# Kernel optimization log

Measured on AMD Instinct MI355X. Metric: run time of the kernel, lower is better.

Reference implementation:

```python
import jax, jax.numpy as jnp
import numpy as np

TEM = 6  # forward hardcodes Tem=6 for index building; init default Tem=6 for weights


def _build_index(H, W, Tem):
    # Faithful port of _build_matrix_index: row edges per phase, col edges per phase,
    # then cross-phase edges linking corresponding pixels of adjacent phases.
    raw = jnp.arange(W, dtype=jnp.int32)[None, :] + jnp.arange(H, dtype=jnp.int32)[:, None] * W  # [H,W]
    pw = W // Tem
    phases = [raw[:, i * pw:(i + 1) * pw] for i in range(Tem)]
    rows = [jnp.stack([p[:-1, :], p[1:, :]], axis=2).reshape(-1, 2) for p in phases]
    cols = [jnp.stack([p[:, :-1], p[:, 1:]], axis=2).reshape(-1, 2) for p in phases]
    cross = [jnp.stack([phases[i], phases[i + 1]], axis=2).reshape(-1, 2) for i in range(Tem - 1)]
    return jnp.concatenate(rows + cols + cross, axis=0)  # [E,2]


def _build_weight_norm2(fm, Tem):
    # Faithful port of _build_feature_weight_norm2_distance, INCLUDING the original
    # per-phase [row,col] interleaved ordering (which differs from the index ordering).
    B, D, H, W = fm.shape
    pw = W // Tem
    phases = [fm[:, :, :, i * pw:(i + 1) * pw] for i in range(Tem)]
    ws = []
    for p in phases:
        wr = ((p[:, :, :-1, :] - p[:, :, 1:, :]) ** 2).sum(axis=1).reshape(B, -1)
        wc = ((p[:, :, :, :-1] - p[:, :, :, 1:]) ** 2).sum(axis=1).reshape(B, -1)
        ws.extend([wr, wc])
    for i in range(Tem - 1):
        ws.append(((phases[i] - phases[i + 1]) ** 2).sum(axis=1).reshape(B, -1))
    return jnp.concatenate(ws, axis=1)  # [B,E]


def _mst_single(u, v, w, V):
    # Vectorized Boruvka MST with pointer-jumping union-find (jit-compatible,
    # fixed round count >= ceil(log2 V)). Ties broken by a globally unique edge rank.
    E = u.shape[0]
    order = jnp.argsort(w)  # stable -> unique rank per edge
    rank = jnp.zeros(E, jnp.int32).at[order].set(jnp.arange(E, dtype=jnp.int32))
    n_rounds = int(np.ceil(np.log2(max(V, 2)))) + 1
    idx_v = jnp.arange(V, dtype=jnp.int32)

    def round_fn(carry, _):
        comp, mask = carry
        cu, cv = comp[u], comp[v]
        active = cu != cv
        key = jnp.where(active, rank, E)  # E = sentinel 'no edge'
        mk = jnp.minimum(jax.ops.segment_min(key, cu, num_segments=V),
                         jax.ops.segment_min(key, cv, num_segments=V))  # min rank per component
        has = mk < E
        sel = order[jnp.clip(mk, 0, E - 1)]  # chosen edge index per component
        a, b = cu[sel], cv[sel]
        other = jnp.where(a == idx_v, b, a)
        parent = jnp.where(has, other, idx_v)
        # break mutual 2-cycles: smaller-index component becomes root
        gp = parent[parent]
        parent = jnp.where((gp == idx_v) & (idx_v < parent), idx_v, parent)
        # full path compression via pointer jumping
        parent = jax.lax.while_loop(lambda p: jnp.any(p[p] != p), lambda p: p[p], parent)
        comp = parent[comp]
        mask = mask.at[jnp.where(has, sel, E)].set(True)  # slot E is scratch
        return (comp, mask), None

    comp0 = jnp.arange(V, dtype=jnp.int32)
    mask0 = jnp.zeros(E + 1, dtype=bool)
    (comp, mask), _ = jax.lax.scan(round_fn, (comp0, mask0), None, length=n_rounds)
    mask = mask[:E]
    # grid graph is connected -> exactly V-1 selected edges; emit sorted edge ids
    tree = jnp.sort(jnp.where(mask, jnp.arange(E, dtype=jnp.int32), E))[: V - 1]
    return tree  # [V-1] int32


def setup_inputs() -> dict:
    key = jax.random.key(0)
    guide_in = jax.random.normal(key, (4, 64, 288, 432), dtype=jnp.float32)
    return {"guide_in": guide_in}


def reference(guide_in):
    B, C, H, W = guide_in.shape
    V = H * W
    index = _build_index(H, W, TEM)  # [E,2], same for every batch element
    weight = _build_weight_norm2(guide_in, TEM)  # [B,E]
    u, v = index[:, 0], index[:, 1]
    tree = jax.vmap(lambda ww: _mst_single(u, v, ww, V))(weight)  # [B, V-1]
    return tree
```

## Files before the change

kernel.cpp:

```cpp
#include <hip/hip_runtime.h>
#include <cstdint>
#include <cstddef>

#define NB 4
#define NC 64
#define HH 288
#define WW 432
#define PW 72
#define NV (HH*WW)
#define R_PER ((HH-1)*PW)
#define C_PER (HH*(PW-1))
#define X_PER (HH*PW)
#define PAIRW (R_PER + C_PER)
#define ROWS_TOT (6*R_PER)
#define ROWCOL (6*PAIRW)
#define NE (ROWCOL + 5*X_PER)
#define NTREE (NV-1)
#define NROUNDS 18
#define CHUNK 4096
#define NCHUNK ((NE + CHUNK - 1)/CHUNK)

typedef unsigned long long ull;

__device__ __forceinline__ void index_uv(int e, int& u, int& v) {
    if (e < ROWS_TOT) {
        int t = e / R_PER, l = e - t * R_PER;
        int h = l / PW, x = l - h * PW;
        u = h * WW + t * PW + x; v = u + WW;
    } else if (e < ROWCOL) {
        int q = e - ROWS_TOT;
        int t = q / C_PER, l = q - t * C_PER;
        int h = l / (PW-1), x = l - h * (PW-1);
        u = h * WW + t * PW + x; v = u + 1;
    } else {
        int q = e - ROWCOL;
        int t = q / X_PER, l = q - t * X_PER;
        int h = l / PW, x = l - h * PW;
        u = h * WW + t * PW + x; v = u + PW;
    }
}

__device__ __forceinline__ void weight_uv(int e, int& a, int& b) {
    if (e < ROWCOL) {
        int t = e / PAIRW, r = e - t * PAIRW;
        if (r < R_PER) {
            int h = r / PW, x = r - h * PW;
            a = h * WW + t * PW + x; b = a + WW;
        } else {
            int r2 = r - R_PER;
            int h = r2 / (PW-1), x = r2 - h * (PW-1);
            a = h * WW + t * PW + x; b = a + 1;
        }
    } else {
        int q = e - ROWCOL;
        int t = q / X_PER, l = q - t * X_PER;
        int h = l / PW, x = l - h * PW;
        a = h * WW + t * PW + x; b = a + PW;
    }
}

__device__ __forceinline__ int rootOf(const int* __restrict__ par, int c) {
    while (true) {
        int p = par[c];
        if (p == c) return c;
        int pp = par[p];
        if (pp == c) return c < p ? c : p;
        c = p;
    }
}

__global__ __launch_bounds__(256) void init_kernel(int* comp, int* parent,
                                                   ull* minkey, unsigned char* mask,
                                                   unsigned char* alive,
                                                   int* foundA, int* foundB, int* done) {
    int i = blockIdx.x * 256 + threadIdx.x;
    int b = blockIdx.y;
    if (i < NV) {
        comp[(size_t)b*NV + i] = i;
        parent[(size_t)b*NV + i] = i;
        minkey[(size_t)b*NV + i] = ~0ULL;
    }
    if (i < NE) {
        mask[(size_t)b*NE + i] = 0;
        alive[(size_t)b*NE + i] = 1;
    }
    if (i == 0) { foundA[b] = 0; foundB[b] = 0; done[b] = 0; }
}

__global__ __launch_bounds__(256) void key_kernel(const float* __restrict__ fm,
                                                  ull* __restrict__ keys) {
    int e = blockIdx.x * 256 + threadIdx.x;
    int b = blockIdx.y;
    if (e >= NE) return;
    int a, c2;
    weight_uv(e, a, c2);
    const float* base = fm + (size_t)b * NC * NV;
    float w = 0.f;
    #pragma unroll 8
    for (int ch = 0; ch < NC; ++ch) {
        float d = base[(size_t)ch * NV + a] - base[(size_t)ch * NV + c2];
        w += d * d;
    }
    keys[(size_t)b * NE + e] =
        ((ull)__float_as_uint(w) << 32) | (unsigned int)e;
}

__global__ __launch_bounds__(256) void scan_kernel(const ull* __restrict__ keys,
                                                   int* __restrict__ comp,
                                                   const int* __restrict__ parent,
                                                   ull* __restrict__ minkey,
                                                   unsigned char* __restrict__ alive,
                                                   int* __restrict__ foundCur,
                                                   const int* __restrict__ done) {
    int e = blockIdx.x * 256 + threadIdx.x;
    int b = blockIdx.y;
    if (e >= NE) return;
    if (done[b]) return;
    if (!alive[(size_t)b * NE + e]) return;
    const int* par = parent + (size_t)b * NV;
    int* cmp = comp + (size_t)b * NV;
    int u, v;
    index_uv(e, u, v);
    int cu = rootOf(par, cmp[u]);
    if (cmp[u] != cu) cmp[u] = cu;
    int cv = rootOf(par, cmp[v]);
    if (cmp[v] != cv) cmp[v] = cv;
    bool pred = (cu != cv);
    if (!pred) alive[(size_t)b * NE + e] = 0;
    ull m = __ballot(pred ? 1 : 0);
    if (m && (threadIdx.x & 63) == (unsigned)(__ffsll((long long)m) - 1))
        foundCur[b] = 1;
    if (pred) {
        ull k = keys[(size_t)b * NE + e];
        ull* mk = minkey + (size_t)b * NV;
        if (k < mk[cu]) atomicMin(&mk[cu], k);
        if (k < mk[cv]) atomicMin(&mk[cv], k);
    }
}

__global__ __launch_bounds__(256) void select_kernel(const int* __restrict__ comp,
                                                     int* __restrict__ parent,
                                                     ull* __restrict__ minkey,
                                                     unsigned char* __restrict__ mask,
                                                     const int* __restrict__ foundCur,
                                                     int* __restrict__ foundNext,
                                                     int* __restrict__ done) {
    int c = blockIdx.x * 256 + threadIdx.x;
    int b = blockIdx.y;
    int fc = foundCur[b];
    if (c == 0) {
        foundNext[b] = 0;
        if (fc == 0) done[b] = 1;
    }
    if (fc == 0) return;
    if (c >= NV) return;
    size_t off = (size_t)b * NV;
    ull k = minkey[off + c];
    int par = c;
    if (k != ~0ULL) {
        minkey[off + c] = ~0ULL;
        int e = (int)(k & 0xffffffffu);
        mask[(size_t)b * NE + e] = 1;
        int u, v;
        index_uv(e, u, v);
        int cu = comp[off + u], cv = comp[off + v];
        par = (cu == c) ? cv : cu;
    }
    if (parent[off + c] != par) parent[off + c] = par;
}

__global__ __launch_bounds__(256) void count_kernel(const unsigned char* __restrict__ mask,
                                                    int* __restrict__ counts) {
    int b = blockIdx.y, ck = blockIdx.x, t = threadIdx.x;
    const unsigned char* m = mask + (size_t)b * NE;
    int base_e = ck * CHUNK + t * 16;
    int cnt = 0;
    #pragma unroll
    for (int i = 0; i < 16; ++i) {
        int e = base_e + i;
        if (e < NE && m[e]) cnt++;
    }
    __shared__ int sh[256];
    sh[t] = cnt;
    __syncthreads();
    for (int o = 128; o > 0; o >>= 1) {
        if (t < o) sh[t] += sh[t + o];
        __syncthreads();
    }
    if (t == 0) counts[b * NCHUNK + ck] = sh[0];
}

__global__ void offs_kernel(const int* __restrict__ counts, int* __restrict__ offsets) {
    int b = threadIdx.x;
    if (b >= NB) return;
    int run = 0;
    for (int ck = 0; ck < NCHUNK; ++ck) {
        int c = counts[b * NCHUNK + ck];
        offsets[b * NCHUNK + ck] = run;
        run += c;
    }
}

__global__ __launch_bounds__(256) void write_kernel(const unsigned char* __restrict__ mask,
                                                    const int* __restrict__ offsets,
                                                    int* __restrict__ out) {
    int b = blockIdx.y, ck = blockIdx.x, t = threadIdx.x;
    const unsigned char* m = mask + (size_t)b * NE;
    int base_e = ck * CHUNK + t * 16;
    int cnt = 0;
    #pragma unroll
    for (int i = 0; i < 16; ++i) {
        int e = base_e + i;
        if (e < NE && m[e]) cnt++;
    }
    __shared__ int sh[256];
    sh[t] = cnt;
    __syncthreads();
    for (int o = 1; o < 256; o <<= 1) {
        int v = 0;
        if (t >= o) v = sh[t - o];
        __syncthreads();
        sh[t] += v;
        __syncthreads();
    }
    int pos = offsets[b * NCHUNK + ck] + (sh[t] - cnt);
    for (int i = 0; i < 16; ++i) {
        int e = base_e + i;
        if (e < NE && m[e]) {
            if (pos < NTREE) out[(size_t)b * NTREE + pos] = e;
            pos++;
        }
    }
}

extern "C" void kernel_launch(void* const* d_in, const int* in_sizes, int n_in,
                              void* d_out, int out_size, void* d_ws, size_t ws_size,
                              hipStream_t stream) {
    const float* fm = (const float*)d_in[0];
    int* out = (int*)d_out;

    char* ws = (char*)d_ws;
    size_t off = 0;
    auto alloc = [&](size_t bytes) -> void* {
        void* p = ws + off;
        off += (bytes + 255) & ~(size_t)255;
        return p;
    };
    ull* keys    = (ull*)alloc((size_t)NB * NE * 8);
    ull* minkey  = (ull*)alloc((size_t)NB * NV * 8);
    int* comp    = (int*)alloc((size_t)NB * NV * 4);
    int* parent  = (int*)alloc((size_t)NB * NV * 4);
    unsigned char* mask  = (unsigned char*)alloc((size_t)NB * NE);
    unsigned char* alive = (unsigned char*)alloc((size_t)NB * NE);
    int* counts  = (int*)alloc((size_t)NB * NCHUNK * 4);
    int* offsets = (int*)alloc((size_t)NB * NCHUNK * 4);
    int* foundA  = (int*)alloc(NB * 4);
    int* foundB  = (int*)alloc(NB * 4);
    int* done    = (int*)alloc(NB * 4);

    dim3 blk(256);
    dim3 gE((NE + 255) / 256, NB);
    dim3 gV((NV + 255) / 256, NB);

    init_kernel<<<gE, blk, 0, stream>>>(comp, parent, minkey, mask, alive,
                                        foundA, foundB, done);
    key_kernel<<<gE, blk, 0, stream>>>(fm, keys);

    for (int r = 0; r < NROUNDS; ++r) {
        int* fCur  = (r & 1) ? foundB : foundA;
        int* fNext = (r & 1) ? foundA : foundB;
        scan_kernel<<<gE, blk, 0, stream>>>(keys, comp, parent, minkey, alive,
                                            fCur, done);
        select_kernel<<<gV, blk, 0, stream>>>(comp, parent, minkey, mask,
                                              fCur, fNext, done);
    }

    count_kernel<<<dim3(NCHUNK, NB), blk, 0, stream>>>(mask, counts);
    offs_kernel<<<1, NB, 0, stream>>>(counts, offsets);
    write_kernel<<<dim3(NCHUNK, NB), blk, 0, stream>>>(mask, offsets, out);
}
```

Measured before the change: 667.4 us.

## Compute edge weights per pixel, fuse first Boruvka scan, bitpack alive flags

The edge-weight kernel now runs once per pixel instead of once per edge, computing the vertical, horizontal and cross-phase distances from one shared center load. This cuts redundant reads of the 64-channel feature map. The same kernel atomically seeds the per-component minimum keys, which replaces the first scan round. The alive flags move from bytes to 32-bit bitmasks written once per wavefront, and the separate offsets kernel is folded into write_kernel as a per-block reduction over the chunk counts. The trade-off is more atomics in the key kernel and a redundant reduction of the counts in every write block.

```diff
diff --git a/kernel.cpp b/kernel.cpp
--- a/kernel.cpp
+++ b/kernel.cpp
@@ -17,6 +17,7 @@
 #define NE (ROWCOL + 5*X_PER)
 #define NTREE (NV-1)
 #define NROUNDS 18
+#define NWORDS ((NE + 31)/32)
 #define CHUNK 4096
 #define NCHUNK ((NE + CHUNK - 1)/CHUNK)
 
@@ -40,25 +41,6 @@
     }
 }
 
-__device__ __forceinline__ void weight_uv(int e, int& a, int& b) {
-    if (e < ROWCOL) {
-        int t = e / PAIRW, r = e - t * PAIRW;
-        if (r < R_PER) {
-            int h = r / PW, x = r - h * PW;
-            a = h * WW + t * PW + x; b = a + WW;
-        } else {
-            int r2 = r - R_PER;
-            int h = r2 / (PW-1), x = r2 - h * (PW-1);
-            a = h * WW + t * PW + x; b = a + 1;
-        }
-    } else {
-        int q = e - ROWCOL;
-        int t = q / X_PER, l = q - t * X_PER;
-        int h = l / PW, x = l - h * PW;
-        a = h * WW + t * PW + x; b = a + PW;
-    }
-}
-
 __device__ __forceinline__ int rootOf(const int* __restrict__ par, int c) {
     while (true) {
         int p = par[c];
@@ -71,8 +53,8 @@
 
 __global__ __launch_bounds__(256) void init_kernel(int* comp, int* parent,
                                                    ull* minkey, unsigned char* mask,
-                                                   unsigned char* alive,
-                                                   int* foundA, int* foundB, int* done) {
+                                                   unsigned* aliveW,
+                                                   int* found, int* done) {
     int i = blockIdx.x * 256 + threadIdx.x;
     int b = blockIdx.y;
     if (i < NV) {
@@ -80,62 +62,99 @@
         parent[(size_t)b*NV + i] = i;
         minkey[(size_t)b*NV + i] = ~0ULL;
     }
-    if (i < NE) {
-        mask[(size_t)b*NE + i] = 0;
-        alive[(size_t)b*NE + i] = 1;
-    }
-    if (i == 0) { foundA[b] = 0; foundB[b] = 0; done[b] = 0; }
-}
-
-__global__ __launch_bounds__(256) void key_kernel(const float* __restrict__ fm,
-                                                  ull* __restrict__ keys) {
-    int e = blockIdx.x * 256 + threadIdx.x;
-    int b = blockIdx.y;
-    if (e >= NE) return;
-    int a, c2;
-    weight_uv(e, a, c2);
-    const float* base = fm + (size_t)b * NC * NV;
-    float w = 0.f;
+    if (i < NE) mask[(size_t)b*NE + i] = 0;
+    if (i < NWORDS) aliveW[(size_t)b*NWORDS + i] = 0xffffffffu;
+    if (b == 0 && i < NB) { found[i] = 1; found[NB + i] = 0; done[i] = 0; }
+}
+
+__global__ __launch_bounds__(256) void key0_kernel(const float* __restrict__ fm,
+                                                   ull* __restrict__ keys,
+                                                   ull* __restrict__ minkey) {
+    int i = blockIdx.x * 256 + threadIdx.x;
+    int b = blockIdx.y;
+    if (i >= NV) return;
+    int h = i / WW, x = i - h * WW;
+    int t = x / PW, xr = x - t * PW;
+    bool hv = (h < HH-1);
+    bool hh = (xr < PW-1);
+    bool hx = (x < WW-PW);
+    int ov = hv ? WW : 0;
+    int oh = hh ? 1  : 0;
+    int ox = hx ? PW : 0;
+    const float* base = fm + (size_t)b * NC * NV + i;
+    float sv = 0.f, sh_ = 0.f, sx = 0.f;
     #pragma unroll 8
     for (int ch = 0; ch < NC; ++ch) {
-        float d = base[(size_t)ch * NV + a] - base[(size_t)ch * NV + c2];
-        w += d * d;
-    }
-    keys[(size_t)b * NE + e] =
-        ((ull)__float_as_uint(w) << 32) | (unsigned int)e;
+        const float* p = base + (size_t)ch * NV;
+        float f0 = p[0];
+        float dv = f0 - p[ov];
+        float dh = f0 - p[oh];
+        float dx = f0 - p[ox];
+        sv += dv * dv; sh_ += dh * dh; sx += dx * dx;
+    }
+    ull* mk = minkey + (size_t)b * NV;
+    ull* ky = keys + (size_t)b * NE;
+    if (hv) {
+        int e = t * PAIRW + h * PW + xr;
+        ull k = ((ull)__float_as_uint(sv) << 32) | (unsigned int)e;
+        ky[e] = k;
+        int u, v; index_uv(e, u, v);
+        atomicMin(&mk[u], k); atomicMin(&mk[v], k);
+    }
+    if (hh) {
+        int e = t * PAIRW + R_PER + h * (PW-1) + xr;
+        ull k = ((ull)__float_as_uint(sh_) << 32) | (unsigned int)e;
+        ky[e] = k;
+        int u, v; index_uv(e, u, v);
+        atomicMin(&mk[u], k); atomicMin(&mk[v], k);
+    }
+    if (hx) {
+        int e = ROWCOL + t * X_PER + h * PW + xr;
+        ull k = ((ull)__float_as_uint(sx) << 32) | (unsigned int)e;
+        ky[e] = k;
+        int u, v; index_uv(e, u, v);
+        atomicMin(&mk[u], k); atomicMin(&mk[v], k);
+    }
 }
 
 __global__ __launch_bounds__(256) void scan_kernel(const ull* __restrict__ keys,
                                                    int* __restrict__ comp,
                                                    const int* __restrict__ parent,
                                                    ull* __restrict__ minkey,
-                                                   unsigned char* __restrict__ alive,
+                                                   unsigned* __restrict__ aliveW,
                                                    int* __restrict__ foundCur,
                                                    const int* __restrict__ done) {
     int e = blockIdx.x * 256 + threadIdx.x;
     int b = blockIdx.y;
-    if (e >= NE) return;
     if (done[b]) return;
-    if (!alive[(size_t)b * NE + e]) return;
-    const int* par = parent + (size_t)b * NV;
-    int* cmp = comp + (size_t)b * NV;
-    int u, v;
-    index_uv(e, u, v);
-    int cu = rootOf(par, cmp[u]);
-    if (cmp[u] != cu) cmp[u] = cu;
-    int cv = rootOf(par, cmp[v]);
-    if (cmp[v] != cv) cmp[v] = cv;
-    bool pred = (cu != cv);
-    if (!pred) alive[(size_t)b * NE + e] = 0;
-    ull m = __ballot(pred ? 1 : 0);
-    if (m && (threadIdx.x & 63) == (unsigned)(__ffsll((long long)m) - 1))
-        foundCur[b] = 1;
-    if (pred) {
+    const int lane = threadIdx.x & 63;
+    unsigned* aw = aliveW + (size_t)b * NWORDS;
+    bool was = false, live = false;
+    int cu = 0, cv = 0;
+    if (e < NE) was = (aw[e >> 5] >> (e & 31)) & 1;
+    if (was) {
+        const int* par = parent + (size_t)b * NV;
+        int* cmp = comp + (size_t)b * NV;
+        int u, v; index_uv(e, u, v);
+        cu = rootOf(par, cmp[u]); if (cmp[u] != cu) cmp[u] = cu;
+        cv = rootOf(par, cmp[v]); if (cmp[v] != cv) cmp[v] = cv;
+        live = (cu != cv);
+    }
+    if (live) {
         ull k = keys[(size_t)b * NE + e];
         ull* mk = minkey + (size_t)b * NV;
         if (k < mk[cu]) atomicMin(&mk[cu], k);
         if (k < mk[cv]) atomicMin(&mk[cv], k);
     }
+    ull ball = __ballot(live ? 1 : 0);
+    ull ballWas = __ballot(was ? 1 : 0);
+    if (ball != ballWas) {
+        int wbase = (blockIdx.x * 256 + (threadIdx.x & ~63)) >> 5;
+        if (lane == 0)  aw[wbase]     = (unsigned)ball;
+        if (lane == 32) aw[wbase + 1] = (unsigned)(ball >> 32);
+    }
+    if (ball && lane == __ffsll((long long)ball) - 1)
+        foundCur[b] = 1;
 }
 
 __global__ __launch_bounds__(256) void select_kernel(const int* __restrict__ comp,
@@ -161,8 +180,7 @@
         minkey[off + c] = ~0ULL;
         int e = (int)(k & 0xffffffffu);
         mask[(size_t)b * NE + e] = 1;
-        int u, v;
-        index_uv(e, u, v);
+        int u, v; index_uv(e, u, v);
         int cu = comp[off + u], cv = comp[off + v];
         par = (cu == c) ? cv : cu;
     }
@@ -190,21 +208,22 @@
     if (t == 0) counts[b * NCHUNK + ck] = sh[0];
 }
 
-__global__ void offs_kernel(const int* __restrict__ counts, int* __restrict__ offsets) {
-    int b = threadIdx.x;
-    if (b >= NB) return;
-    int run = 0;
-    for (int ck = 0; ck < NCHUNK; ++ck) {
-        int c = counts[b * NCHUNK + ck];
-        offsets[b * NCHUNK + ck] = run;
-        run += c;
-    }
-}
-
 __global__ __launch_bounds__(256) void write_kernel(const unsigned char* __restrict__ mask,
-                                                    const int* __restrict__ offsets,
+                                                    const int* __restrict__ counts,
                                                     int* __restrict__ out) {
     int b = blockIdx.y, ck = blockIdx.x, t = threadIdx.x;
+    __shared__ int sh[256];
+    __shared__ int shOff[128];
+    shOff[t & 127] = 0;
+    __syncthreads();
+    if (t < NCHUNK && t < ck) shOff[t] = counts[b * NCHUNK + t];
+    __syncthreads();
+    for (int o = 64; o > 0; o >>= 1) {
+        if (t < o) shOff[t] += shOff[t + o];
+        __syncthreads();
+    }
+    int blockOff = shOff[0];
+
     const unsigned char* m = mask + (size_t)b * NE;
     int base_e = ck * CHUNK + t * 16;
     int cnt = 0;
@@ -213,7 +232,6 @@
         int e = base_e + i;
         if (e < NE && m[e]) cnt++;
     }
-    __shared__ int sh[256];
     sh[t] = cnt;
     __syncthreads();
     for (int o = 1; o < 256; o <<= 1) {
@@ -223,7 +241,7 @@
         sh[t] += v;
         __syncthreads();
     }
-    int pos = offsets[b * NCHUNK + ck] + (sh[t] - cnt);
+    int pos = blockOff + (sh[t] - cnt);
     for (int i = 0; i < 16; ++i) {
         int e = base_e + i;
         if (e < NE && m[e]) {
@@ -250,32 +268,30 @@
     ull* minkey  = (ull*)alloc((size_t)NB * NV * 8);
     int* comp    = (int*)alloc((size_t)NB * NV * 4);
     int* parent  = (int*)alloc((size_t)NB * NV * 4);
-    unsigned char* mask  = (unsigned char*)alloc((size_t)NB * NE);
-    unsigned char* alive = (unsigned char*)alloc((size_t)NB * NE);
+    unsigned char* mask = (unsigned char*)alloc((size_t)NB * NE);
+    unsigned* aliveW = (unsigned*)alloc((size_t)NB * NWORDS * 4);
     int* counts  = (int*)alloc((size_t)NB * NCHUNK * 4);
-    int* offsets = (int*)alloc((size_t)NB * NCHUNK * 4);
-    int* foundA  = (int*)alloc(NB * 4);
-    int* foundB  = (int*)alloc(NB * 4);
+    int* found   = (int*)alloc(2 * NB * 4);
     int* done    = (int*)alloc(NB * 4);
 
     dim3 blk(256);
     dim3 gE((NE + 255) / 256, NB);
     dim3 gV((NV + 255) / 256, NB);
 
-    init_kernel<<<gE, blk, 0, stream>>>(comp, parent, minkey, mask, alive,
-                                        foundA, foundB, done);
-    key_kernel<<<gE, blk, 0, stream>>>(fm, keys);
-
-    for (int r = 0; r < NROUNDS; ++r) {
-        int* fCur  = (r & 1) ? foundB : foundA;
-        int* fNext = (r & 1) ? foundA : foundB;
-        scan_kernel<<<gE, blk, 0, stream>>>(keys, comp, parent, minkey, alive,
+    init_kernel<<<gE, blk, 0, stream>>>(comp, parent, minkey, mask, aliveW, found, done);
+    key0_kernel<<<gV, blk, 0, stream>>>(fm, keys, minkey);
+
+    select_kernel<<<gV, blk, 0, stream>>>(comp, parent, minkey, mask,
+                                          found, found + NB, done);
+    for (int r = 1; r < NROUNDS; ++r) {
+        int* fCur  = found + (r & 1) * NB;
+        int* fNext = found + ((r + 1) & 1) * NB;
+        scan_kernel<<<gE, blk, 0, stream>>>(keys, comp, parent, minkey, aliveW,
                                             fCur, done);
         select_kernel<<<gV, blk, 0, stream>>>(comp, parent, minkey, mask,
                                               fCur, fNext, done);
     }
 
     count_kernel<<<dim3(NCHUNK, NB), blk, 0, stream>>>(mask, counts);
-    offs_kernel<<<1, NB, 0, stream>>>(counts, offsets);
-    write_kernel<<<dim3(NCHUNK, NB), blk, 0, stream>>>(mask, offsets, out);
-}
+    write_kernel<<<dim3(NCHUNK, NB), blk, 0, stream>>>(mask, counts, out);
+}
```

Result: faster. 633.4 us (-5.1%).
